# Optimization experiments

Hardware: AMD Instinct MI355X
Metric: run time of the kernel (lower is better)

The kernel has to match this reference:

```python
import jax, jax.numpy as jnp
import numpy as np

NUM_HEADS = 16
NEG_INF = -1e30  # finite large negative; avoids NaN on fully-masked padded query rows


def setup_inputs() -> dict:
    key = jax.random.key(0)
    k0, k1, k2, k3 = jax.random.split(key, 4)
    B, S, E = 4, 2048, 1024
    x_padded = jax.random.normal(k0, (B, S, E), dtype=jnp.float32)
    # variable lengths in [S//2, S] so no batch row is fully empty
    seq_lengths = jax.random.randint(k1, (B,), S // 2, S + 1).astype(jnp.int32)
    Wqkv = jax.random.normal(k2, (3 * E, E), dtype=jnp.float32) * 0.02  # torch Linear weight [out,in]
    Wout = jax.random.normal(k3, (E, E), dtype=jnp.float32) * 0.02
    return {"x_padded": x_padded, "Wqkv": Wqkv, "Wout": Wout,
            "seq_lengths": seq_lengths, "window_left": 512, "window_right": 0}


def _build_mask(seq_lengths, S, window_left, window_right):
    # key-side padding mask: [B, S]
    pad = jnp.arange(S)[None, :] < seq_lengths[:, None]
    mask = pad[:, None, None, :]  # [B,1,1,S]
    if window_left >= 0 or window_right >= 0:
        i = jnp.arange(S)[:, None]
        j = jnp.arange(S)[None, :]
        win = jnp.ones((S, S), dtype=bool)
        if window_left >= 0:
            win = win & (j >= i - window_left)
        if window_right >= 0:
            win = win & (j <= i + window_right)
        mask = mask & win[None, None, :, :]
    elif (window_left, window_right) == (-1, 0):
        causal = jnp.tril(jnp.ones((S, S), dtype=bool))
        mask = mask & causal[None, None, :, :]
    return mask  # [B,1,S,S] (broadcasts over heads)


def reference(x_padded, Wqkv, Wout, seq_lengths, window_left, window_right):
    B, S, E = x_padded.shape
    H = NUM_HEADS
    D = E // H
    scale = 1.0 / jnp.sqrt(jnp.float32(D))
    qkv = x_padded @ Wqkv.T  # [B,S,3E]
    q, k, v = jnp.split(qkv, 3, axis=-1)
    q = q.reshape(B, S, H, D).transpose(0, 2, 1, 3)  # [B,H,S,D]
    k = k.reshape(B, S, H, D).transpose(0, 2, 1, 3)
    v = v.reshape(B, S, H, D).transpose(0, 2, 1, 3)
    mask = _build_mask(seq_lengths, S, window_left, window_right)
    scores = jnp.einsum("bhid,bhjd->bhij", q, k) * scale
    scores = jnp.where(mask, scores, NEG_INF)
    attn = jax.nn.softmax(scores, axis=-1)
    out = jnp.einsum("bhij,bhjd->bhid", attn, v)  # [B,H,S,D]
    out = out.transpose(0, 2, 1, 3).reshape(B, S, E)
    return out @ Wout.T
```

## Files before the change

### kernel.cpp

```cpp
#include <hip/hip_runtime.h>

typedef __bf16 bf16;
typedef __attribute__((ext_vector_type(2))) __bf16 bf16x2;
typedef __attribute__((ext_vector_type(4))) __bf16 bf16x4;
typedef __attribute__((ext_vector_type(8))) __bf16 bf16x8;
typedef __attribute__((ext_vector_type(4))) float f32x4;
typedef __attribute__((ext_vector_type(16))) float f32x16;

#define B_ 4
#define S_ 2048
#define H_ 16
#define D_ 64
#define E_ 1024

#define BM 256
#define BN 128
#define BK 64

__device__ __forceinline__ int imin(int a, int b) { return a < b ? a : b; }
__device__ __forceinline__ int imax(int a, int b) { return a > b ? a : b; }

__device__ __forceinline__ void gload_lds16(const void* g, void* l) {
  __builtin_amdgcn_global_load_lds(
      (const __attribute__((address_space(1))) void*)g,
      (__attribute__((address_space(3))) void*)l, 16, 0, 0);
}

__global__ __launch_bounds__(256) void f32_to_bf16_kernel(
    const float* __restrict__ in, bf16* __restrict__ out, int n) {
  int i = (blockIdx.x * 256 + threadIdx.x) * 8;
  const int stride = gridDim.x * 256 * 8;
  for (; i < n; i += stride) {
    float4 v0 = *(const float4*)(in + i);
    float4 v1 = *(const float4*)(in + i + 4);
    bf16x8 o;
    o[0] = (bf16)v0.x; o[1] = (bf16)v0.y; o[2] = (bf16)v0.z; o[3] = (bf16)v0.w;
    o[4] = (bf16)v1.x; o[5] = (bf16)v1.y; o[6] = (bf16)v1.z; o[7] = (bf16)v1.w;
    *(bf16x8*)(out + i) = o;
  }
}

__global__ __launch_bounds__(512, 1) void gemm_pipe(
    const bf16* __restrict__ A, const bf16* __restrict__ Bm,
    int M, int N, int K, int mode,
    bf16* __restrict__ qd, bf16* __restrict__ kd, bf16* __restrict__ vtd,
    float* __restrict__ outf) {
  __shared__ __align__(16) bf16 As[3][BM * BK];
  __shared__ __align__(16) bf16 Bs[3][BN * BK];
  const int tid = threadIdx.x;
  const int wave = tid >> 6, lane = tid & 63;
  const int l15 = lane & 15, l4 = lane >> 4;
  const int wm = (wave >> 1) * 64;
  const int wn = (wave & 1) * 64;

  const int nwg = gridDim.x * gridDim.y;
  const int fid = blockIdx.y * gridDim.x + blockIdx.x;
  const int chunk = nwg >> 3;
  const int swz = (fid & 7) * chunk + (fid >> 3);
  const int tn = swz % gridDim.x;
  const int tm = swz / gridDim.x;

  const bf16* Abase = A + (size_t)tm * BM * K;
  const bf16* Bbase = Bm + (size_t)tn * BN * K;

  f32x4 acc[4][4];
#pragma unroll
  for (int i = 0; i < 4; ++i)
#pragma unroll
    for (int j = 0; j < 4; ++j)
#pragma unroll
      for (int r = 0; r < 4; ++r) acc[i][j][r] = 0.f;

  const int NT = K >> 6;

#define STAGE_A(sbuf, k0)                                                      \
  {                                                                            \
    _Pragma("unroll") for (int ld = 0; ld < 4; ++ld) {                         \
      const int idx = ld * 512 + tid;                                          \
      const int row = idx >> 3, g = idx & 7;                                   \
      const int gs = g ^ (row & 7);                                            \
      gload_lds16(Abase + (size_t)row * K + (k0) + gs * 8,                     \
                  As[sbuf] + (ld * 512 + wave * 64) * 8);                      \
    }                                                                          \
  }
#define STAGE_B(sbuf, k0)                                                      \
  {                                                                            \
    _Pragma("unroll") for (int ld = 0; ld < 2; ++ld) {                         \
      const int idx = ld * 512 + tid;                                          \
      const int row = idx >> 3, g = idx & 7;                                   \
      const int gs = g ^ (row & 7);                                            \
      gload_lds16(Bbase + (size_t)row * K + (k0) + gs * 8,                     \
                  Bs[sbuf] + (ld * 512 + wave * 64) * 8);                      \
    }                                                                          \
  }

  STAGE_A(0, 0); STAGE_B(0, 0);
  STAGE_A(1, BK); STAGE_B(1, BK);
  asm volatile("s_waitcnt vmcnt(6)" ::: "memory");
  __builtin_amdgcn_s_barrier();

  int p = 0;
  for (int t = 0; t < NT; ++t) {
    const bf16* Ap = As[p];
    const bf16* Bp = Bs[p];
    const int sb = (p + 2 >= 3) ? p - 1 : p + 2;
    const int sk0 = ((t + 2 < NT) ? t + 2 : NT - 1) * BK;

    bf16x8 a[4], bfr[4];
#pragma unroll
    for (int i = 0; i < 4; ++i) {
      const int ra = wm + i * 16 + l15;
      a[i] = *(const bf16x8*)(Ap + ra * 64 + ((l4 ^ (ra & 7)) * 8));
      const int rb = wn + i * 16 + l15;
      bfr[i] = *(const bf16x8*)(Bp + rb * 64 + ((l4 ^ (rb & 7)) * 8));
    }
    STAGE_A(sb, sk0);
    __builtin_amdgcn_s_setprio(1);
#pragma unroll
    for (int i = 0; i < 4; ++i)
#pragma unroll
      for (int j = 0; j < 4; ++j)
        acc[i][j] = __builtin_amdgcn_mfma_f32_16x16x32_bf16(a[i], bfr[j],
                                                            acc[i][j], 0, 0, 0);
    __builtin_amdgcn_s_setprio(0);
#pragma unroll
    for (int i = 0; i < 4; ++i) {
      const int ra = wm + i * 16 + l15;
      a[i] = *(const bf16x8*)(Ap + ra * 64 + (((4 + l4) ^ (ra & 7)) * 8));
      const int rb = wn + i * 16 + l15;
      bfr[i] = *(const bf16x8*)(Bp + rb * 64 + (((4 + l4) ^ (rb & 7)) * 8));
    }
    STAGE_B(sb, sk0);
    __builtin_amdgcn_s_setprio(1);
#pragma unroll
    for (int i = 0; i < 4; ++i)
#pragma unroll
      for (int j = 0; j < 4; ++j)
        acc[i][j] = __builtin_amdgcn_mfma_f32_16x16x32_bf16(a[i], bfr[j],
                                                            acc[i][j], 0, 0, 0);
    __builtin_amdgcn_s_setprio(0);

    asm volatile("s_waitcnt vmcnt(6)" ::: "memory");
    __builtin_amdgcn_s_barrier();
    p = (p + 1 >= 3) ? 0 : p + 1;
  }
#undef STAGE_A
#undef STAGE_B

  if (mode == 0) {
#pragma unroll
    for (int i = 0; i < 4; ++i) {
      const int m0 = tm * BM + wm + i * 16 + l4 * 4;
      const int b = m0 >> 11, s = m0 & (S_ - 1);
#pragma unroll
      for (int j = 0; j < 4; ++j) {
        const int n = tn * BN + wn + j * 16 + l15;
        const int which = n >> 10;
        const int hn = n & 1023;
        const int h = hn >> 6, d = hn & 63;
        const f32x4 av = acc[i][j];
        if (which == 0) {
#pragma unroll
          for (int r = 0; r < 4; ++r)
            qd[((size_t)(b * H_ + h) * S_ + (s + r)) * D_ + d] =
                (bf16)(av[r] * 0.125f);
        } else if (which == 1) {
#pragma unroll
          for (int r = 0; r < 4; ++r)
            kd[((size_t)(b * H_ + h) * S_ + (s + r)) * D_ + d] = (bf16)av[r];
        } else {
          bf16x4 pv;
#pragma unroll
          for (int r = 0; r < 4; ++r) pv[r] = (bf16)av[r];
          *(bf16x4*)(vtd + ((size_t)(b * H_ + h) * D_ + d) * S_ + s) = pv;
        }
      }
    }
  } else {
#pragma unroll
    for (int i = 0; i < 4; ++i) {
      const int m0 = tm * BM + wm + i * 16 + l4 * 4;
#pragma unroll
      for (int j = 0; j < 4; ++j) {
        const int n = tn * BN + wn + j * 16 + l15;
#pragma unroll
        for (int r = 0; r < 4; ++r) outf[(size_t)(m0 + r) * N + n] = acc[i][j][r];
      }
    }
  }
}

__global__ __launch_bounds__(256) void meanv_kernel(const bf16* __restrict__ vt,
                                                    float* __restrict__ meanv) {
  __shared__ float part[256];
  const int bh = blockIdx.x;
  const int tid = threadIdx.x;
  const int d = tid & 63, seg = tid >> 6;
  const bf16* row = vt + ((size_t)bh * D_ + d) * S_ + seg * 512;
  float s = 0.f;
  for (int i = 0; i < 512; i += 8) {
    bf16x8 v = *(const bf16x8*)(row + i);
#pragma unroll
    for (int j = 0; j < 8; ++j) s += (float)v[j];
  }
  part[tid] = s;
  __syncthreads();
  if (tid < 64) {
    float t = part[tid] + part[64 + tid] + part[128 + tid] + part[192 + tid];
    meanv[(size_t)bh * D_ + tid] = t * (1.0f / (float)S_);
  }
}

__device__ __forceinline__ int pk2(float a, float b) {
  union { bf16x2 h; int i; } u;
  u.h[0] = (bf16)a; u.h[1] = (bf16)b;
  return u.i;
}

__global__ __launch_bounds__(256) void attn_kernel(
    const bf16* __restrict__ q, const bf16* __restrict__ k,
    const bf16* __restrict__ vt, const float* __restrict__ meanv,
    const int* __restrict__ seq_lengths, const int* __restrict__ wlp,
    const int* __restrict__ wrp, bf16* __restrict__ attn_out) {
  __shared__ __align__(16) bf16 Ks[2][64 * 64];
  __shared__ __align__(16) bf16 Vs[2][64 * 64];
  const int tid = threadIdx.x, wave = tid >> 6, lane = tid & 63;
  const int l31 = lane & 31, l5 = lane >> 5;
  const int bid0 = blockIdx.x;
  const int bid = (bid0 & 7) * 128 + (bid0 >> 3);
  const int bh = bid >> 4;
  const int g = bid & 15;
  const int b = bh >> 4, h = bh & 15;
  const int q0b = g * 128;
  const int q0w = q0b + wave * 32;
  const int seq_len = seq_lengths[b];
  const int wl = wlp[0], wr = wrp[0];

  const bf16* qbase = q + (size_t)bh * S_ * D_;
  const bf16* kbase = k + (size_t)bh * S_ * D_;
  const bf16* vtb = vt + (size_t)bh * D_ * S_;

  bf16x8 qa[4];
#pragma unroll
  for (int dg = 0; dg < 4; ++dg)
    qa[dg] = *(const bf16x8*)(qbase + (size_t)(q0w + l31) * D_ + dg * 16 + l5 * 8);

  const int hi_blk = (wr >= 0) ? imin(q0b + 127 + wr, S_ - 1) : (S_ - 1);
  const int end_blk = imin(hi_blk + 1, seq_len);
  const int lo_blk = (wl >= 0) ? imax(0, q0b - wl) : 0;
  const int beg_blk = lo_blk & ~63;
  const int ntb = (end_blk > beg_blk) ? ((end_blk - beg_blk + 63) >> 6) : 0;

  const int w_hi = (wr >= 0) ? (q0w + 31 + wr) : (S_ - 1);
  const int w_end = imin(w_hi + 1, seq_len);
  const int w_lo = (wl >= 0) ? imax(0, q0w - wl) : 0;

  f32x16 o0, o1;
#pragma unroll
  for (int r = 0; r < 16; ++r) { o0[r] = 0.f; o1[r] = 0.f; }
  float mrun = -1e30f, lrun = 0.f;

#define STAGE(bufb, kt0)                                                       \
  {                                                                            \
    _Pragma("unroll") for (int ld = 0; ld < 2; ++ld) {                         \
      const int idx = ld * 256 + tid;                                          \
      const int row = idx >> 3, gg = idx & 7;                                  \
      const int gs = gg ^ (row & 7);                                           \
      const int krow = imin((kt0) + row, S_ - 1);                              \
      gload_lds16(kbase + (size_t)krow * 64 + gs * 8, Ks[bufb] + idx * 8);     \
      const int vcol = imin((kt0) + gs * 8, S_ - 8);                           \
      gload_lds16(vtb + (size_t)row * S_ + vcol, Vs[bufb] + idx * 8);          \
    }                                                                          \
  }
#define LDS_K(bufb, row, gran)                                                 \
  (*(const bf16x8*)((const char*)(Ks[bufb]) + (row) * 128 +                    \
                    (((gran) ^ ((row) & 7)) << 4)))
#define LDS_V(bufb, row, gran)                                                 \
  (*(const bf16x8*)((const char*)(Vs[bufb]) + (row) * 128 +                    \
                    (((gran) ^ ((row) & 7)) << 4)))

  if (ntb > 0) STAGE(0, beg_blk);
  __syncthreads();

  for (int t = 0; t < ntb; ++t) {
    const int kt = beg_blk + t * 64;
    if (t + 1 < ntb) STAGE((t + 1) & 1, kt + 64);

    const bool active = (kt < w_end) && (kt + 63 >= w_lo);
    if (active) {
      const int bufb = t & 1;
      f32x16 sf0, sf1;
#pragma unroll
      for (int r = 0; r < 16; ++r) { sf0[r] = 0.f; sf1[r] = 0.f; }
#pragma unroll
      for (int dg = 0; dg < 4; ++dg) {
        bf16x8 kb0 = LDS_K(bufb, l31, dg * 2 + l5);
        bf16x8 kb1 = LDS_K(bufb, 32 + l31, dg * 2 + l5);
        sf0 = __builtin_amdgcn_mfma_f32_32x32x16_bf16(kb0, qa[dg], sf0, 0, 0, 0);
        sf1 = __builtin_amdgcn_mfma_f32_32x32x16_bf16(kb1, qa[dg], sf1, 0, 0, 0);
      }

      bool allv = (kt + 63 < seq_len);
      if (wr >= 0) allv = allv && (kt + 63 <= q0w + wr);
      if (wl >= 0) allv = allv && (kt >= q0w + 31 - wl);
      if (!allv) {
        const int qrow = q0w + l31;
#pragma unroll
        for (int hh = 0; hh < 2; ++hh)
#pragma unroll
          for (int r = 0; r < 16; ++r) {
            const int key = kt + hh * 32 + (r & 3) + 8 * (r >> 2) + 4 * l5;
            bool valid = (key < seq_len);
            if (wr >= 0) valid = valid && (key <= qrow + wr);
            if (wl >= 0) valid = valid && (key >= qrow - wl);
            if (hh == 0) sf0[r] = valid ? sf0[r] : -1e30f;
            else sf1[r] = valid ? sf1[r] : -1e30f;
          }
      }
      float tmax = -1e30f;
#pragma unroll
      for (int r = 0; r < 16; ++r) {
        tmax = fmaxf(tmax, sf0[r]);
        tmax = fmaxf(tmax, sf1[r]);
      }
      tmax = fmaxf(tmax, __shfl_xor(tmax, 32, 64));

      if (!__all(tmax <= mrun + 8.0f)) {
        const float mnew = fmaxf(mrun, tmax);
        const float corr = __expf(mrun - mnew);
        mrun = mnew;
        lrun *= corr;
#pragma unroll
        for (int r = 0; r < 16; ++r) { o0[r] *= corr; o1[r] *= corr; }
      }

      float lsum = 0.f;
#pragma unroll
      for (int r = 0; r < 16; ++r) {
        const float e0 = (sf0[r] <= -1e29f) ? 0.f : __expf(sf0[r] - mrun);
        const float e1 = (sf1[r] <= -1e29f) ? 0.f : __expf(sf1[r] - mrun);
        sf0[r] = e0; sf1[r] = e1;
        lsum += e0 + e1;
      }
      lsum += __shfl_xor(lsum, 32, 64);
      lrun += lsum;

      bf16x8 pb[4];
#pragma unroll
      for (int kg = 0; kg < 4; ++kg) {
        const int base = (kg & 1) * 8;
        float p0, p1, p2, p3, p4, p5, p6, p7;
        if (kg < 2) {
          p0 = sf0[base + 0]; p1 = sf0[base + 1]; p2 = sf0[base + 2];
          p3 = sf0[base + 3]; p4 = sf0[base + 4]; p5 = sf0[base + 5];
          p6 = sf0[base + 6]; p7 = sf0[base + 7];
        } else {
          p0 = sf1[base + 0]; p1 = sf1[base + 1]; p2 = sf1[base + 2];
          p3 = sf1[base + 3]; p4 = sf1[base + 4]; p5 = sf1[base + 5];
          p6 = sf1[base + 6]; p7 = sf1[base + 7];
        }
        const int w0 = pk2(p0, p1);
        const int w1 = pk2(p2, p3);
        const int w2 = pk2(p4, p5);
        const int w3 = pk2(p6, p7);
        auto r02 = __builtin_amdgcn_permlane32_swap(w0, w2, false, false);
        auto r13 = __builtin_amdgcn_permlane32_swap(w1, w3, false, false);
        union { int i[4]; bf16x8 v; } u;
        u.i[0] = r02[0]; u.i[1] = r13[0]; u.i[2] = r02[1]; u.i[3] = r13[1];
        pb[kg] = u.v;
      }

#pragma unroll
      for (int kg = 0; kg < 4; ++kg) {
        bf16x8 va0 = LDS_V(bufb, l31, kg * 2 + l5);
        bf16x8 va1 = LDS_V(bufb, 32 + l31, kg * 2 + l5);
        o0 = __builtin_amdgcn_mfma_f32_32x32x16_bf16(va0, pb[kg], o0, 0, 0, 0);
        o1 = __builtin_amdgcn_mfma_f32_32x32x16_bf16(va1, pb[kg], o1, 0, 0, 0);
      }
    }
    __syncthreads();
  }
#undef STAGE
#undef LDS_K
#undef LDS_V

  const int qrow = q0w + l31;
  bf16* outp = attn_out + ((size_t)(b * S_ + qrow)) * E_ + h * 64;
  if (lrun > 0.f) {
    const float inv = 1.0f / lrun;
#pragma unroll
    for (int dg2 = 0; dg2 < 2; ++dg2) {
      const f32x16& o = dg2 ? o1 : o0;
#pragma unroll
      for (int rg = 0; rg < 4; ++rg) {
        const int d0 = dg2 * 32 + 8 * rg + 4 * l5;
        bf16x4 ov;
#pragma unroll
        for (int j = 0; j < 4; ++j) ov[j] = (bf16)(o[rg * 4 + j] * inv);
        *(bf16x4*)(outp + d0) = ov;
      }
    }
  } else {
    const float* mv = meanv + (size_t)bh * D_;
#pragma unroll
    for (int dg2 = 0; dg2 < 2; ++dg2)
#pragma unroll
      for (int rg = 0; rg < 4; ++rg) {
        const int d0 = dg2 * 32 + 8 * rg + 4 * l5;
        bf16x4 ov;
#pragma unroll
        for (int j = 0; j < 4; ++j) ov[j] = (bf16)mv[d0 + j];
        *(bf16x4*)(outp + d0) = ov;
      }
  }
}

extern "C" void kernel_launch(void* const* d_in, const int* in_sizes, int n_in,
                              void* d_out, int out_size, void* d_ws, size_t ws_size,
                              hipStream_t stream) {
  const float* x = (const float*)d_in[0];
  const float* Wqkv = (const float*)d_in[1];
  const float* Wout = (const float*)d_in[2];
  const int* seq_lengths = (const int*)d_in[3];
  const int* wl = (const int*)d_in[4];
  const int* wr = (const int*)d_in[5];
  float* out = (float*)d_out;

  char* ws = (char*)d_ws;
  bf16* xb = (bf16*)ws;      ws += (size_t)8192 * 1024 * 2;
  bf16* wqkvb = (bf16*)ws;   ws += (size_t)3072 * 1024 * 2;
  bf16* woutb = (bf16*)ws;   ws += (size_t)1024 * 1024 * 2;
  bf16* qd = (bf16*)ws;      ws += (size_t)B_ * H_ * S_ * D_ * 2;
  bf16* kd = (bf16*)ws;      ws += (size_t)B_ * H_ * S_ * D_ * 2;
  bf16* vtd = (bf16*)ws;     ws += (size_t)B_ * H_ * S_ * D_ * 2;
  bf16* attn = (bf16*)ws;    ws += (size_t)8192 * 1024 * 2;
  float* meanv = (float*)ws; ws += (size_t)B_ * H_ * D_ * 4;

  f32_to_bf16_kernel<<<2048, 256, 0, stream>>>(x, xb, 8192 * 1024);
  f32_to_bf16_kernel<<<768, 256, 0, stream>>>(Wqkv, wqkvb, 3072 * 1024);
  f32_to_bf16_kernel<<<512, 256, 0, stream>>>(Wout, woutb, 1024 * 1024);

  gemm_pipe<<<dim3(24, 32), 512, 0, stream>>>(xb, wqkvb, 8192, 3072, 1024, 0,
                                              qd, kd, vtd, nullptr);
  meanv_kernel<<<64, 256, 0, stream>>>(vtd, meanv);
  attn_kernel<<<1024, 256, 0, stream>>>(qd, kd, vtd, meanv, seq_lengths, wl, wr,
                                        attn);
  gemm_pipe<<<dim3(8, 32), 512, 0, stream>>>(attn, woutb, 8192, 1024, 1024, 1,
                                             nullptr, nullptr, nullptr, out);
}
```

Measured before the change: 177.6 us.

## Restructure GEMM to 128x256x32 tiles with 4 waves and two blocks per CU

Replaces the 512-thread 256x128x64 GEMM with a 256-thread kernel using 128x256 tiles and K-step 32. Each wave now owns a 64-column strip across all 128 rows, and the swizzle pattern and staging are adapted to match. Launch bounds allow two workgroups per CU for better latency hiding. Extra barriers are added inside each K iteration, and the smaller K step doubles the iteration count, adding sync overhead.

```diff
diff --git a/kernel.cpp b/kernel.cpp
--- a/kernel.cpp
+++ b/kernel.cpp
@@ -13,9 +13,9 @@
 #define D_ 64
 #define E_ 1024
 
-#define BM 256
-#define BN 128
-#define BK 64
+#define QBM 128
+#define QBN 256
+#define QBK 32
 
 __device__ __forceinline__ int imin(int a, int b) { return a < b ? a : b; }
 __device__ __forceinline__ int imax(int a, int b) { return a > b ? a : b; }
@@ -40,18 +40,16 @@
   }
 }
 
-__global__ __launch_bounds__(512, 1) void gemm_pipe(
+__global__ __launch_bounds__(256, 2) void gemm_q(
     const bf16* __restrict__ A, const bf16* __restrict__ Bm,
-    int M, int N, int K, int mode,
+    int K, int mode, int N,
     bf16* __restrict__ qd, bf16* __restrict__ kd, bf16* __restrict__ vtd,
     float* __restrict__ outf) {
-  __shared__ __align__(16) bf16 As[3][BM * BK];
-  __shared__ __align__(16) bf16 Bs[3][BN * BK];
+  __shared__ __align__(16) bf16 As[3][QBM * QBK];
+  __shared__ __align__(16) bf16 Bs[3][QBN * QBK];
   const int tid = threadIdx.x;
   const int wave = tid >> 6, lane = tid & 63;
   const int l15 = lane & 15, l4 = lane >> 4;
-  const int wm = (wave >> 1) * 64;
-  const int wn = (wave & 1) * 64;
 
   const int nwg = gridDim.x * gridDim.y;
   const int fid = blockIdx.y * gridDim.x + blockIdx.x;
@@ -60,133 +58,146 @@
   const int tn = swz % gridDim.x;
   const int tm = swz / gridDim.x;
 
-  const bf16* Abase = A + (size_t)tm * BM * K;
-  const bf16* Bbase = Bm + (size_t)tn * BN * K;
-
-  f32x4 acc[4][4];
-#pragma unroll
-  for (int i = 0; i < 4; ++i)
+  const bf16* Abase = A + (size_t)tm * QBM * K;
+  const bf16* Bbase = Bm + (size_t)tn * QBN * K;
+
+  f32x4 acc[8][4];
+#pragma unroll
+  for (int i = 0; i < 8; ++i)
 #pragma unroll
     for (int j = 0; j < 4; ++j)
 #pragma unroll
       for (int r = 0; r < 4; ++r) acc[i][j][r] = 0.f;
 
-  const int NT = K >> 6;
-
-#define STAGE_A(sbuf, k0)                                                      \
+  const int NT = K >> 5;
+
+#define QSTG_A(buf, k0, ld)                                                    \
   {                                                                            \
-    _Pragma("unroll") for (int ld = 0; ld < 4; ++ld) {                         \
-      const int idx = ld * 512 + tid;                                          \
-      const int row = idx >> 3, g = idx & 7;                                   \
-      const int gs = g ^ (row & 7);                                            \
-      gload_lds16(Abase + (size_t)row * K + (k0) + gs * 8,                     \
-                  As[sbuf] + (ld * 512 + wave * 64) * 8);                      \
-    }                                                                          \
-  }
-#define STAGE_B(sbuf, k0)                                                      \
+    const int idx = (ld) * 256 + tid;                                          \
+    const int row = idx >> 2, g = idx & 3;                                     \
+    const int gs = g ^ ((row >> 1) & 3);                                       \
+    gload_lds16(Abase + (size_t)row * K + (k0) + gs * 8,                       \
+                As[buf] + ((ld) * 256 + wave * 64) * 8);                       \
+  }
+#define QSTG_B(buf, k0, ld)                                                    \
   {                                                                            \
-    _Pragma("unroll") for (int ld = 0; ld < 2; ++ld) {                         \
-      const int idx = ld * 512 + tid;                                          \
-      const int row = idx >> 3, g = idx & 7;                                   \
-      const int gs = g ^ (row & 7);                                            \
-      gload_lds16(Bbase + (size_t)row * K + (k0) + gs * 8,                     \
-                  Bs[sbuf] + (ld * 512 + wave * 64) * 8);                      \
-    }                                                                          \
-  }
-
-  STAGE_A(0, 0); STAGE_B(0, 0);
-  STAGE_A(1, BK); STAGE_B(1, BK);
+    const int idx = (ld) * 256 + tid;                                          \
+    const int row = idx >> 2, g = idx & 3;                                     \
+    const int gs = g ^ ((row >> 1) & 3);                                       \
+    gload_lds16(Bbase + (size_t)row * K + (k0) + gs * 8,                       \
+                Bs[buf] + ((ld) * 256 + wave * 64) * 8);                       \
+  }
+#define QRD_A(buf, r)                                                          \
+  (*(const bf16x8*)((const char*)As[buf] + (size_t)(r) * 64 +                  \
+                    ((l4 ^ (((r) >> 1) & 3)) << 4)))
+#define QRD_B(buf, r)                                                          \
+  (*(const bf16x8*)((const char*)Bs[buf] + (size_t)(r) * 64 +                  \
+                    ((l4 ^ (((r) >> 1) & 3)) << 4)))
+
+  QSTG_A(0, 0, 0) QSTG_A(0, 0, 1)
+  QSTG_B(0, 0, 0) QSTG_B(0, 0, 1) QSTG_B(0, 0, 2) QSTG_B(0, 0, 3)
+  QSTG_A(1, QBK, 0) QSTG_A(1, QBK, 1)
+  QSTG_B(1, QBK, 0) QSTG_B(1, QBK, 1) QSTG_B(1, QBK, 2) QSTG_B(1, QBK, 3)
   asm volatile("s_waitcnt vmcnt(6)" ::: "memory");
   __builtin_amdgcn_s_barrier();
 
   int p = 0;
   for (int t = 0; t < NT; ++t) {
-    const bf16* Ap = As[p];
-    const bf16* Bp = Bs[p];
     const int sb = (p + 2 >= 3) ? p - 1 : p + 2;
-    const int sk0 = ((t + 2 < NT) ? t + 2 : NT - 1) * BK;
-
-    bf16x8 a[4], bfr[4];
-#pragma unroll
-    for (int i = 0; i < 4; ++i) {
-      const int ra = wm + i * 16 + l15;
-      a[i] = *(const bf16x8*)(Ap + ra * 64 + ((l4 ^ (ra & 7)) * 8));
-      const int rb = wn + i * 16 + l15;
-      bfr[i] = *(const bf16x8*)(Bp + rb * 64 + ((l4 ^ (rb & 7)) * 8));
+    const int sk = ((t + 2 < NT) ? t + 2 : NT - 1) * QBK;
+
+    bf16x8 af[4], bq0[2], bq1[2];
+#pragma unroll
+    for (int mi = 0; mi < 4; ++mi) af[mi] = QRD_A(p, mi * 16 + l15);
+#pragma unroll
+    for (int nj = 0; nj < 2; ++nj) {
+      bq0[nj] = QRD_B(p, wave * 64 + nj * 16 + l15);
+      bq1[nj] = QRD_B(p, wave * 64 + 32 + nj * 16 + l15);
     }
-    STAGE_A(sb, sk0);
+    QSTG_A(sb, sk, 0) QSTG_A(sb, sk, 1) QSTG_B(sb, sk, 0)
+    __builtin_amdgcn_s_barrier();
     __builtin_amdgcn_s_setprio(1);
 #pragma unroll
-    for (int i = 0; i < 4; ++i)
-#pragma unroll
-      for (int j = 0; j < 4; ++j)
-        acc[i][j] = __builtin_amdgcn_mfma_f32_16x16x32_bf16(a[i], bfr[j],
-                                                            acc[i][j], 0, 0, 0);
+    for (int mi = 0; mi < 4; ++mi)
+#pragma unroll
+      for (int nj = 0; nj < 2; ++nj) {
+        acc[mi][nj] = __builtin_amdgcn_mfma_f32_16x16x32_bf16(
+            af[mi], bq0[nj], acc[mi][nj], 0, 0, 0);
+        acc[mi][2 + nj] = __builtin_amdgcn_mfma_f32_16x16x32_bf16(
+            af[mi], bq1[nj], acc[mi][2 + nj], 0, 0, 0);
+      }
     __builtin_amdgcn_s_setprio(0);
-#pragma unroll
-    for (int i = 0; i < 4; ++i) {
-      const int ra = wm + i * 16 + l15;
-      a[i] = *(const bf16x8*)(Ap + ra * 64 + (((4 + l4) ^ (ra & 7)) * 8));
-      const int rb = wn + i * 16 + l15;
-      bfr[i] = *(const bf16x8*)(Bp + rb * 64 + (((4 + l4) ^ (rb & 7)) * 8));
-    }
-    STAGE_B(sb, sk0);
+
+#pragma unroll
+    for (int mi = 0; mi < 4; ++mi) af[mi] = QRD_A(p, 64 + mi * 16 + l15);
+    QSTG_B(sb, sk, 1) QSTG_B(sb, sk, 2) QSTG_B(sb, sk, 3)
+    __builtin_amdgcn_s_barrier();
     __builtin_amdgcn_s_setprio(1);
 #pragma unroll
-    for (int i = 0; i < 4; ++i)
-#pragma unroll
-      for (int j = 0; j < 4; ++j)
-        acc[i][j] = __builtin_amdgcn_mfma_f32_16x16x32_bf16(a[i], bfr[j],
-                                                            acc[i][j], 0, 0, 0);
+    for (int mi = 0; mi < 4; ++mi)
+#pragma unroll
+      for (int nj = 0; nj < 2; ++nj) {
+        acc[4 + mi][nj] = __builtin_amdgcn_mfma_f32_16x16x32_bf16(
+            af[mi], bq0[nj], acc[4 + mi][nj], 0, 0, 0);
+        acc[4 + mi][2 + nj] = __builtin_amdgcn_mfma_f32_16x16x32_bf16(
+            af[mi], bq1[nj], acc[4 + mi][2 + nj], 0, 0, 0);
+      }
     __builtin_amdgcn_s_setprio(0);
 
     asm volatile("s_waitcnt vmcnt(6)" ::: "memory");
     __builtin_amdgcn_s_barrier();
     p = (p + 1 >= 3) ? 0 : p + 1;
   }
-#undef STAGE_A
-#undef STAGE_B
+#undef QSTG_A
+#undef QSTG_B
+#undef QRD_A
+#undef QRD_B
 
   if (mode == 0) {
 #pragma unroll
-    for (int i = 0; i < 4; ++i) {
-      const int m0 = tm * BM + wm + i * 16 + l4 * 4;
-      const int b = m0 >> 11, s = m0 & (S_ - 1);
-#pragma unroll
-      for (int j = 0; j < 4; ++j) {
-        const int n = tn * BN + wn + j * 16 + l15;
-        const int which = n >> 10;
-        const int hn = n & 1023;
-        const int h = hn >> 6, d = hn & 63;
-        const f32x4 av = acc[i][j];
-        if (which == 0) {
+    for (int ms = 0; ms < 2; ++ms)
+#pragma unroll
+      for (int mi = 0; mi < 4; ++mi) {
+        const int m0 = tm * QBM + ms * 64 + mi * 16 + l4 * 4;
+        const int b = m0 >> 11, s = m0 & (S_ - 1);
+#pragma unroll
+        for (int nc = 0; nc < 4; ++nc) {
+          const int n = tn * QBN + wave * 64 + (nc >> 1) * 32 + (nc & 1) * 16 + l15;
+          const int which = n >> 10;
+          const int hn = n & 1023;
+          const int h = hn >> 6, d = hn & 63;
+          const f32x4 av = acc[ms * 4 + mi][nc];
+          if (which == 0) {
+#pragma unroll
+            for (int r = 0; r < 4; ++r)
+              qd[((size_t)(b * H_ + h) * S_ + (s + r)) * D_ + d] =
+                  (bf16)(av[r] * 0.125f);
+          } else if (which == 1) {
+#pragma unroll
+            for (int r = 0; r < 4; ++r)
+              kd[((size_t)(b * H_ + h) * S_ + (s + r)) * D_ + d] = (bf16)av[r];
+          } else {
+            bf16x4 pv;
+#pragma unroll
+            for (int r = 0; r < 4; ++r) pv[r] = (bf16)av[r];
+            *(bf16x4*)(vtd + ((size_t)(b * H_ + h) * D_ + d) * S_ + s) = pv;
+          }
+        }
+      }
+  } else {
+#pragma unroll
+    for (int ms = 0; ms < 2; ++ms)
+#pragma unroll
+      for (int mi = 0; mi < 4; ++mi) {
+        const int m0 = tm * QBM + ms * 64 + mi * 16 + l4 * 4;
+#pragma unroll
+        for (int nc = 0; nc < 4; ++nc) {
+          const int n = tn * QBN + wave * 64 + (nc >> 1) * 32 + (nc & 1) * 16 + l15;
 #pragma unroll
           for (int r = 0; r < 4; ++r)
-            qd[((size_t)(b * H_ + h) * S_ + (s + r)) * D_ + d] =
-                (bf16)(av[r] * 0.125f);
-        } else if (which == 1) {
-#pragma unroll
-          for (int r = 0; r < 4; ++r)
-            kd[((size_t)(b * H_ + h) * S_ + (s + r)) * D_ + d] = (bf16)av[r];
-        } else {
-          bf16x4 pv;
-#pragma unroll
-          for (int r = 0; r < 4; ++r) pv[r] = (bf16)av[r];
-          *(bf16x4*)(vtd + ((size_t)(b * H_ + h) * D_ + d) * S_ + s) = pv;
+            outf[(size_t)(m0 + r) * N + n] = acc[ms * 4 + mi][nc][r];
         }
       }
-    }
-  } else {
-#pragma unroll
-    for (int i = 0; i < 4; ++i) {
-      const int m0 = tm * BM + wm + i * 16 + l4 * 4;
-#pragma unroll
-      for (int j = 0; j < 4; ++j) {
-        const int n = tn * BN + wn + j * 16 + l15;
-#pragma unroll
-        for (int r = 0; r < 4; ++r) outf[(size_t)(m0 + r) * N + n] = acc[i][j][r];
-      }
-    }
   }
 }
 
@@ -440,11 +451,11 @@
   f32_to_bf16_kernel<<<768, 256, 0, stream>>>(Wqkv, wqkvb, 3072 * 1024);
   f32_to_bf16_kernel<<<512, 256, 0, stream>>>(Wout, woutb, 1024 * 1024);
 
-  gemm_pipe<<<dim3(24, 32), 512, 0, stream>>>(xb, wqkvb, 8192, 3072, 1024, 0,
-                                              qd, kd, vtd, nullptr);
+  gemm_q<<<dim3(12, 64), 256, 0, stream>>>(xb, wqkvb, 1024, 0, 3072,
+                                           qd, kd, vtd, nullptr);
   meanv_kernel<<<64, 256, 0, stream>>>(vtd, meanv);
   attn_kernel<<<1024, 256, 0, stream>>>(qd, kd, vtd, meanv, seq_lengths, wl, wr,
                                         attn);
-  gemm_pipe<<<dim3(8, 32), 512, 0, stream>>>(attn, woutb, 8192, 1024, 1024, 1,
-                                             nullptr, nullptr, nullptr, out);
-}
+  gemm_q<<<dim3(4, 64), 256, 0, stream>>>(attn, woutb, 1024, 1, 1024,
+                                          nullptr, nullptr, nullptr, out);
+}
```

Result: slower. 194.6 us (+9.6%).
